# Kernel tuning notes

Measured on AMD Instinct MI355X. Metric: run time of the kernel, lower is better.

Reference implementation:

```python
import jax, jax.numpy as jnp
import numpy as np

MD_R = 64          # low-rank R
NMF_STEPS = 7      # EVAL_STEPS
INV_T = 1.0
EPS = 1e-6
GN_GROUPS = 32


def _nmf_step(x, bases, coef):
    # x: (B,D,N), bases: (B,D,R), coef: (B,N,R) -- multiplicative NMF updates
    btb = jnp.einsum('bdr,bdk->brk', bases, bases)                 # (B,R,R)
    coef = coef * jnp.einsum('bdn,bdr->bnr', x, bases) / (
        jnp.einsum('bnr,brk->bnk', coef, btb) + EPS)
    ctc = jnp.einsum('bnr,bnk->brk', coef, coef)                   # (B,R,R)
    bases = bases * jnp.einsum('bdn,bnr->bdr', x, coef) / (
        jnp.einsum('bdr,brk->bdk', bases, ctc) + EPS)
    return bases, coef


def setup_inputs() -> dict:
    key = jax.random.key(0)
    ks = jax.random.split(key, 7)
    B, C, H, W = 8, 256, 64, 64
    x = jax.random.normal(ks[0], (B, C, H, W), jnp.float32)
    w_in = jax.random.normal(ks[1], (C, C), jnp.float32) * 0.02
    b_in = jnp.zeros((C,), jnp.float32)
    w_out = jax.random.normal(ks[2], (C, C), jnp.float32) * 0.02
    gn_gamma = jnp.ones((C,), jnp.float32)
    gn_beta = jnp.zeros((C,), jnp.float32)
    bases_init = jax.random.uniform(ks[3], (B, C, MD_R), jnp.float32)  # RAND_INIT bases
    return {"x": x, "w_in": w_in, "b_in": b_in, "w_out": w_out,
            "gn_gamma": gn_gamma, "gn_beta": gn_beta, "bases_init": bases_init}


def reference(x, w_in, b_in, w_out, gn_gamma, gn_beta, bases_init):
    B, C, H, W = x.shape
    N = H * W
    # ham_in: 1x1 conv with bias, then relu
    h = jnp.einsum('bchw,oc->bohw', x, w_in) + b_in[None, :, None, None]
    h = jax.nn.relu(h)
    # NMF2D: flatten spatial (SPATIAL=True, S=1 -> D=C)
    xm = h.reshape(B, C, N)                                         # (B,D,N)
    # F.normalize(rand bases, dim=1)
    bases = bases_init / jnp.maximum(
        jnp.linalg.norm(bases_init, axis=1, keepdims=True), 1e-12)
    # local_inference runs under no_grad in the original; math identical here
    xs = jax.lax.stop_gradient(xm)
    coef = jax.nn.softmax(INV_T * jnp.einsum('bdn,bdr->bnr', xs, bases), axis=-1)
    for _ in range(NMF_STEPS):
        bases, coef = _nmf_step(xs, bases, coef)
    bases = jax.lax.stop_gradient(bases)
    coef = jax.lax.stop_gradient(coef)
    # compute_coef (differentiable w.r.t. xm)
    btb = jnp.einsum('bdr,bdk->brk', bases, bases)
    coef = coef * jnp.einsum('bdn,bdr->bnr', xm, bases) / (
        jnp.einsum('bnr,brk->bnk', coef, btb) + EPS)
    rec = jnp.einsum('bdr,bnr->bdn', bases, coef).reshape(B, C, H, W)
    # ham_out: 1x1 conv (no bias) + GroupNorm(32)
    o = jnp.einsum('bchw,oc->bohw', rec, w_out)
    g = o.reshape(B, GN_GROUPS, C // GN_GROUPS, H, W)
    mu = g.mean(axis=(2, 3, 4), keepdims=True)
    var = g.var(axis=(2, 3, 4), keepdims=True)
    g = (g - mu) * jax.lax.rsqrt(var + 1e-5)
    o = g.reshape(B, C, H, W) * gn_gamma[None, :, None, None] + gn_beta[None, :, None, None]
    # residual + relu
    return jax.nn.relu(x + o)
```

## Files before the change

kernel.cpp:

```cpp
#include <hip/hip_runtime.h>

#define B_ 8
#define C_ 256
#define N_ 4096
#define R_ 64
#define STEPS_ 7
#define NCH_ 128
#define NSP_ 32
#define EPS_ 1e-6f

typedef unsigned short u16;
typedef short bf8v __attribute__((ext_vector_type(8)));
typedef float f4v __attribute__((ext_vector_type(4)));

#define MFMA(a, b, c) __builtin_amdgcn_mfma_f32_16x16x32_bf16((a), (b), (c), 0, 0, 0)

__device__ __forceinline__ u16 bf(float x) {
  union { float f; unsigned u; } v; v.f = x;
  return (u16)((v.u + 0x7FFFu + ((v.u >> 16) & 1u)) >> 16);
}
__device__ __forceinline__ float bf2f(u16 x) {
  union { unsigned u; float f; } v; v.u = (unsigned)x << 16; return v.f;
}
__device__ __forceinline__ bf8v ldf(const u16* p) { return *(const bf8v*)p; }

__global__ __launch_bounds__(256)
void prep_kernel(const float* __restrict__ binit, float* __restrict__ bases,
                 u16* __restrict__ basesT,
                 const float* __restrict__ w1, const float* __restrict__ w2,
                 u16* __restrict__ w1b, u16* __restrict__ w2b) {
  const int t = threadIdx.x;
  if (blockIdx.x >= 8) {
    const int i = (blockIdx.x - 8) * 256 + t;
    w1b[i] = bf(w1[i]);
    w2b[i] = bf(w2[i]);
    return;
  }
  const int b = blockIdx.x;
  const int rr = t & 63, dq = t >> 6;
  const float* src = binit + (size_t)b * C_ * R_;
  float* dst = bases + (size_t)b * C_ * R_;
  u16* dT  = basesT + (size_t)b * R_ * C_;
  float vals[64];
  float s = 0.f;
#pragma unroll
  for (int i = 0; i < 64; ++i) {
    float v = src[(size_t)(dq + 4 * i) * R_ + rr];
    vals[i] = v; s = fmaf(v, v, s);
  }
  __shared__ float red[4][64];
  red[dq][rr] = s;
  __syncthreads();
  float nrm = fmaxf(sqrtf(red[0][rr] + red[1][rr] + red[2][rr] + red[3][rr]), 1e-12f);
  const float inv = 1.f / nrm;
#pragma unroll
  for (int i = 0; i < 64; ++i) {
    const int d = dq + 4 * i;
    const float v = vals[i] * inv;
    dst[(size_t)d * R_ + rr] = v;
    dT[(size_t)rr * C_ + d]  = bf(v);
  }
}

__global__ __launch_bounds__(256)
void xpose_kernel(const float* __restrict__ x, u16* __restrict__ xT) {
  const int n0 = blockIdx.x * 64, c0 = blockIdx.y * 64, b = blockIdx.z;
  __shared__ float lds[64][65];
  const int t = threadIdx.x;
  const float* xb = x + (size_t)b * C_ * N_;
  const int row = t >> 4, col4 = (t & 15) * 4;
#pragma unroll
  for (int p = 0; p < 4; ++p) {
    float4 v = *(const float4*)&xb[(size_t)(c0 + row + 16 * p) * N_ + n0 + col4];
    lds[row + 16 * p][col4 + 0] = v.x; lds[row + 16 * p][col4 + 1] = v.y;
    lds[row + 16 * p][col4 + 2] = v.z; lds[row + 16 * p][col4 + 3] = v.w;
  }
  __syncthreads();
  const int r = t >> 2, cb = (t & 3) * 16;
  __align__(16) u16 tmp[16];
#pragma unroll
  for (int j = 0; j < 16; ++j) tmp[j] = bf(lds[cb + j][r]);
  u16* o = xT + (size_t)b * N_ * C_ + (size_t)(n0 + r) * C_ + c0 + cb;
  *(uint4*)o = *(uint4*)tmp;
  *(uint4*)(o + 8) = *(uint4*)(tmp + 8);
}

__global__ __launch_bounds__(256)
void conv1_kernel(const u16* __restrict__ A, const u16* __restrict__ W,
                  const float* __restrict__ bias, u16* __restrict__ h_dn,
                  u16* __restrict__ h_nd) {
  const int nb0 = blockIdx.x * 128, ob0 = blockIdx.y * 128, b = blockIdx.z;
  const int t = threadIdx.x, w = t >> 6, lane = t & 63, g = lane >> 4, c = lane & 15;
  const int n_base = nb0 + (w >> 1) * 64, o_base = ob0 + (w & 1) * 64;
  const u16* Ab = A + (size_t)b * N_ * C_;
  f4v acc[4][4] = {};
  for (int k0 = 0; k0 < C_; k0 += 32) {
    bf8v av[4], wv[4];
#pragma unroll
    for (int mi = 0; mi < 4; ++mi)
      av[mi] = ldf(Ab + (size_t)(n_base + mi * 16 + c) * C_ + k0 + g * 8);
#pragma unroll
    for (int nj = 0; nj < 4; ++nj)
      wv[nj] = ldf(W + (size_t)(o_base + nj * 16 + c) * C_ + k0 + g * 8);
#pragma unroll
    for (int mi = 0; mi < 4; ++mi)
#pragma unroll
      for (int nj = 0; nj < 4; ++nj)
        acc[mi][nj] = MFMA(av[mi], wv[nj], acc[mi][nj]);
  }
  __shared__ float lds[64][65];
  for (int p = 0; p < 4; ++p) {
    if (w == p) {
#pragma unroll
      for (int mi = 0; mi < 4; ++mi)
#pragma unroll
        for (int nj = 0; nj < 4; ++nj) {
          const float bb = bias[o_base + nj * 16 + c];
#pragma unroll
          for (int rg = 0; rg < 4; ++rg)
            lds[mi * 16 + g * 4 + rg][nj * 16 + c] = fmaxf(acc[mi][nj][rg] + bb, 0.f);
        }
    }
    __syncthreads();
    const int pn = nb0 + (p >> 1) * 64, po = ob0 + (p & 1) * 64;
    {
      const int n = t >> 2, ob2 = (t & 3) * 16;
      __align__(16) u16 tmp[16];
#pragma unroll
      for (int j = 0; j < 16; ++j) tmp[j] = bf(lds[n][ob2 + j]);
      u16* o = h_nd + (size_t)b * N_ * C_ + (size_t)(pn + n) * C_ + po + ob2;
      *(uint4*)o = *(uint4*)tmp; *(uint4*)(o + 8) = *(uint4*)(tmp + 8);
    }
    {
      const int oo = t >> 2, nb2 = (t & 3) * 16;
      __align__(16) u16 tmp[16];
#pragma unroll
      for (int j = 0; j < 16; ++j) tmp[j] = bf(lds[nb2 + j][oo]);
      u16* o = h_dn + (size_t)b * C_ * N_ + (size_t)(po + oo) * N_ + pn + nb2;
      *(uint4*)o = *(uint4*)tmp; *(uint4*)(o + 8) = *(uint4*)(tmp + 8);
    }
    __syncthreads();
  }
}

template<int MODE>
__global__ __launch_bounds__(512)
void nmf_kernel(const u16* __restrict__ h_nd, const u16* __restrict__ h_dn,
                const u16* __restrict__ basesT, const u16* __restrict__ w2b,
                u16* __restrict__ coef_bf, u16* __restrict__ m2_bf,
                float* __restrict__ ctcp, float* __restrict__ xcp) {
  const int nc0 = blockIdx.x * NCH_;
  const int b = blockIdx.y;
  const int t = threadIdx.x, w = t >> 6, lane = t & 63, g = lane >> 4, c = lane & 15;
  __shared__ u16 bT_s[64 * 256];
  __shared__ u16 btb_s[64][72];
  __shared__ u16 coef_s[128][72];
  __shared__ u16 coefT_s[64][136];
  const u16* hb = h_nd + (size_t)b * N_ * C_;
  const u16* bT = basesT + (size_t)b * R_ * C_;
  u16* cb = coef_bf + (size_t)b * N_ * R_;

#pragma unroll
  for (int i = 0; i < 4; ++i) {
    const int lin = t + i * 512;
    const int r = lin >> 5, k = lin & 31;
    *(uint4*)&bT_s[r * 256 + ((k ^ (r & 7)) * 8)] =
        *(const uint4*)&bT[(size_t)r * C_ + k * 8];
  }
  if (MODE != 0) {
    const int row = t >> 2, seg = (t & 3) * 16;
    const u16* src = cb + (size_t)(nc0 + row) * R_ + seg;
    *(uint4*)&coef_s[row][seg] = *(const uint4*)src;
    *(uint4*)&coef_s[row][seg + 8] = *(const uint4*)(src + 8);
  }
  __syncthreads();

  const int nl = w * 16 + c;

  f4v num[4] = {}, bt[4] = {};
  const u16* An = hb + (size_t)(nc0 + nl) * C_;
  for (int k0 = 0; k0 < C_; k0 += 32) {
    const int kc = (k0 >> 3) + g;
    bf8v bv[4];
#pragma unroll
    for (int nj = 0; nj < 4; ++nj)
      bv[nj] = *(const bf8v*)&bT_s[(nj * 16 + c) * 256 + ((kc ^ (c & 7)) * 8)];
    bf8v a = ldf(An + k0 + g * 8);
#pragma unroll
    for (int nj = 0; nj < 4; ++nj) num[nj] = MFMA(a, bv[nj], num[nj]);
    if (w < 4) {
      bf8v a2 = *(const bf8v*)&bT_s[(w * 16 + c) * 256 + ((kc ^ (c & 7)) * 8)];
#pragma unroll
      for (int nj = 0; nj < 4; ++nj) bt[nj] = MFMA(a2, bv[nj], bt[nj]);
    }
  }

  if (MODE == 0) {
#pragma unroll
    for (int rg = 0; rg < 4; ++rg) {
      float m = fmaxf(fmaxf(num[0][rg], num[1][rg]), fmaxf(num[2][rg], num[3][rg]));
#pragma unroll
      for (int off = 1; off < 16; off <<= 1) m = fmaxf(m, __shfl_xor(m, off));
      float e[4], s = 0.f;
#pragma unroll
      for (int nj = 0; nj < 4; ++nj) { e[nj] = __expf(num[nj][rg] - m); s += e[nj]; }
#pragma unroll
      for (int off = 1; off < 16; off <<= 1) s += __shfl_xor(s, off);
      const float inv = 1.f / s;
#pragma unroll
      for (int nj = 0; nj < 4; ++nj)
        coef_s[w * 16 + g * 4 + rg][nj * 16 + c] = bf(e[nj] * inv);
    }
  }

  if (w < 4) {
#pragma unroll
    for (int nj = 0; nj < 4; ++nj)
#pragma unroll
      for (int rg = 0; rg < 4; ++rg)
        btb_s[w * 16 + g * 4 + rg][nj * 16 + c] = bf(bt[nj][rg]);
  }
  __syncthreads();

  f4v den[4] = {};
#pragma unroll
  for (int k0 = 0; k0 < R_; k0 += 32) {
    bf8v a = *(const bf8v*)&coef_s[nl][k0 + g * 8];
#pragma unroll
    for (int nj = 0; nj < 4; ++nj)
      den[nj] = MFMA(a, *(const bf8v*)&btb_s[nj * 16 + c][k0 + g * 8], den[nj]);
  }
  __syncthreads();

#pragma unroll
  for (int nj = 0; nj < 4; ++nj)
#pragma unroll
    for (int rg = 0; rg < 4; ++rg) {
      const int row = w * 16 + g * 4 + rg, r = nj * 16 + c;
      const float old = bf2f(coef_s[row][r]);
      const u16 nv = bf(old * num[nj][rg] / (den[nj][rg] + EPS_));
      coef_s[row][r] = nv;
      if (MODE <= 1) coefT_s[r][row] = nv;
    }
  __syncthreads();

  {
    const int row = t >> 2, seg = (t & 3) * 16;
    u16* dst = cb + (size_t)(nc0 + row) * R_ + seg;
    *(uint4*)dst = *(const uint4*)&coef_s[row][seg];
    *(uint4*)(dst + 8) = *(const uint4*)&coef_s[row][seg + 8];
  }

  if (MODE <= 1) {
    f4v xa[2][4] = {};
    const u16* hd = h_dn + (size_t)b * C_ * N_;
    for (int k0 = 0; k0 < NCH_; k0 += 32) {
      bf8v bv[4];
#pragma unroll
      for (int nj = 0; nj < 4; ++nj)
        bv[nj] = *(const bf8v*)&coefT_s[nj * 16 + c][k0 + g * 8];
#pragma unroll
      for (int mi = 0; mi < 2; ++mi) {
        bf8v a = ldf(hd + (size_t)(w * 32 + mi * 16 + c) * N_ + nc0 + k0 + g * 8);
#pragma unroll
        for (int nj = 0; nj < 4; ++nj) xa[mi][nj] = MFMA(a, bv[nj], xa[mi][nj]);
      }
    }
    float* xo = xcp + ((size_t)b * NSP_ + blockIdx.x) * (C_ * R_);
#pragma unroll
    for (int mi = 0; mi < 2; ++mi)
#pragma unroll
      for (int nj = 0; nj < 4; ++nj)
#pragma unroll
        for (int rg = 0; rg < 4; ++rg)
          xo[(size_t)(w * 32 + mi * 16 + g * 4 + rg) * R_ + nj * 16 + c] = xa[mi][nj][rg];
    if (w < 4) {
      f4v ca[4] = {};
      for (int k0 = 0; k0 < NCH_; k0 += 32) {
        bf8v a = *(const bf8v*)&coefT_s[w * 16 + c][k0 + g * 8];
#pragma unroll
        for (int nj = 0; nj < 4; ++nj)
          ca[nj] = MFMA(a, *(const bf8v*)&coefT_s[nj * 16 + c][k0 + g * 8], ca[nj]);
      }
      float* co = ctcp + ((size_t)b * NSP_ + blockIdx.x) * (R_ * R_);
#pragma unroll
      for (int nj = 0; nj < 4; ++nj)
#pragma unroll
        for (int rg = 0; rg < 4; ++rg)
          co[(size_t)(w * 16 + g * 4 + rg) * R_ + nj * 16 + c] = ca[nj][rg];
    }
  }

  if (MODE == 2 && blockIdx.x == 0) {
    f4v ma[2][4] = {};
    for (int k0 = 0; k0 < C_; k0 += 32) {
      const int kc = (k0 >> 3) + g;
      bf8v bv[4];
#pragma unroll
      for (int nj = 0; nj < 4; ++nj)
        bv[nj] = *(const bf8v*)&bT_s[(nj * 16 + c) * 256 + ((kc ^ (c & 7)) * 8)];
#pragma unroll
      for (int mi = 0; mi < 2; ++mi) {
        bf8v a = ldf(w2b + (size_t)(w * 32 + mi * 16 + c) * C_ + k0 + g * 8);
#pragma unroll
        for (int nj = 0; nj < 4; ++nj) ma[mi][nj] = MFMA(a, bv[nj], ma[mi][nj]);
      }
    }
    u16* mo = m2_bf + (size_t)b * C_ * R_;
#pragma unroll
    for (int mi = 0; mi < 2; ++mi)
#pragma unroll
      for (int nj = 0; nj < 4; ++nj)
#pragma unroll
        for (int rg = 0; rg < 4; ++rg)
          mo[(size_t)(w * 32 + mi * 16 + g * 4 + rg) * R_ + nj * 16 + c] = bf(ma[mi][nj][rg]);
  }
}

__global__ __launch_bounds__(256)
void bases_update_kernel(const float* __restrict__ xcp, const float* __restrict__ ctcp,
                         float* __restrict__ bases, u16* __restrict__ basesT) {
  const int dt = blockIdx.x & 3, rt = blockIdx.x >> 2, b = blockIdx.y;
  const int d0 = dt * 64, rb = rt * 16;
  float* bb = bases + (size_t)b * C_ * R_;
  __shared__ float ctc_s[64][16];
  __shared__ float b_s[64][65];
  const int t = threadIdx.x;
  {
    const int k = t >> 2, cr = (t & 3) * 4;
    float4 a = make_float4(0, 0, 0, 0);
    for (int s = 0; s < NSP_; ++s) {
      float4 v = *(const float4*)&ctcp[((size_t)b * NSP_ + s) * (R_ * R_) + (size_t)k * R_ + rb + cr];
      a.x += v.x; a.y += v.y; a.z += v.z; a.w += v.w;
    }
    *(float4*)&ctc_s[k][cr] = a;
  }
  {
    const int lc = t & 63, lr = t >> 6;
#pragma unroll
    for (int p = 0; p < 16; ++p)
      b_s[lr + 4 * p][lc] = bb[(size_t)(d0 + lr + 4 * p) * R_ + lc];
  }
  __syncthreads();
  const int dd = t >> 2, r0 = rb + (t & 3) * 4, cr = (t & 3) * 4;
  float4 num2 = make_float4(0, 0, 0, 0);
  for (int s = 0; s < NSP_; ++s) {
    float4 v = *(const float4*)&xcp[(((size_t)b * NSP_ + s) * C_ + d0 + dd) * R_ + r0];
    num2.x += v.x; num2.y += v.y; num2.z += v.z; num2.w += v.w;
  }
  float4 den = make_float4(0, 0, 0, 0);
#pragma unroll
  for (int k = 0; k < 64; ++k) {
    const float a = b_s[dd][k];
    float4 cv = *(const float4*)&ctc_s[k][cr];
    den.x = fmaf(a, cv.x, den.x); den.y = fmaf(a, cv.y, den.y);
    den.z = fmaf(a, cv.z, den.z); den.w = fmaf(a, cv.w, den.w);
  }
  float4 o;
  o.x = b_s[dd][r0 + 0] * num2.x / (den.x + EPS_);
  o.y = b_s[dd][r0 + 1] * num2.y / (den.y + EPS_);
  o.z = b_s[dd][r0 + 2] * num2.z / (den.z + EPS_);
  o.w = b_s[dd][r0 + 3] * num2.w / (den.w + EPS_);
  *(float4*)&bb[(size_t)(d0 + dd) * R_ + r0] = o;
  u16* oT = basesT + (size_t)b * R_ * C_ + d0 + dd;
  oT[(size_t)(r0 + 0) * C_] = bf(o.x); oT[(size_t)(r0 + 1) * C_] = bf(o.y);
  oT[(size_t)(r0 + 2) * C_] = bf(o.z); oT[(size_t)(r0 + 3) * C_] = bf(o.w);
}

__global__ __launch_bounds__(256)
void conv2_kernel(const u16* __restrict__ coef, const u16* __restrict__ m2,
                  float* __restrict__ of32, float* __restrict__ pstats) {
  const int nb0 = blockIdx.x * 128, ob0 = blockIdx.y * 128, b = blockIdx.z;
  const int t = threadIdx.x, w = t >> 6, lane = t & 63, g = lane >> 4, c = lane & 15;
  const int n_base = nb0 + (w >> 1) * 64, o_base = ob0 + (w & 1) * 64;
  const u16* Ab = coef + (size_t)b * N_ * R_;
  const u16* Wb = m2 + (size_t)b * C_ * R_;
  f4v acc[4][4] = {};
#pragma unroll
  for (int k0 = 0; k0 < R_; k0 += 32) {
    bf8v av[4], wv[4];
#pragma unroll
    for (int mi = 0; mi < 4; ++mi)
      av[mi] = ldf(Ab + (size_t)(n_base + mi * 16 + c) * R_ + k0 + g * 8);
#pragma unroll
    for (int nj = 0; nj < 4; ++nj)
      wv[nj] = ldf(Wb + (size_t)(o_base + nj * 16 + c) * R_ + k0 + g * 8);
#pragma unroll
    for (int mi = 0; mi < 4; ++mi)
#pragma unroll
      for (int nj = 0; nj < 4; ++nj)
        acc[mi][nj] = MFMA(av[mi], wv[nj], acc[mi][nj]);
  }
  __shared__ float lds[64][65];
  float sacc0 = 0.f, sacc1 = 0.f, s2acc0 = 0.f, s2acc1 = 0.f;
  for (int p = 0; p < 4; ++p) {
    if (w == p) {
#pragma unroll
      for (int mi = 0; mi < 4; ++mi)
#pragma unroll
        for (int nj = 0; nj < 4; ++nj)
#pragma unroll
          for (int rg = 0; rg < 4; ++rg)
            lds[mi * 16 + g * 4 + rg][nj * 16 + c] = acc[mi][nj][rg];
    }
    __syncthreads();
    const int pn = nb0 + (p >> 1) * 64, po = ob0 + (p & 1) * 64;
    const int oo = t >> 2, nb2 = (t & 3) * 16;
    float* o = of32 + (size_t)b * C_ * N_ + (size_t)(po + oo) * N_ + pn + nb2;
    float ls = 0.f, ls2 = 0.f;
#pragma unroll
    for (int q = 0; q < 4; ++q) {
      float4 v = make_float4(lds[nb2 + q * 4 + 0][oo], lds[nb2 + q * 4 + 1][oo],
                             lds[nb2 + q * 4 + 2][oo], lds[nb2 + q * 4 + 3][oo]);
      *(float4*)&o[q * 4] = v;
      ls += v.x + v.y + v.z + v.w;
      ls2 = fmaf(v.x, v.x, ls2); ls2 = fmaf(v.y, v.y, ls2);
      ls2 = fmaf(v.z, v.z, ls2); ls2 = fmaf(v.w, v.w, ls2);
    }
    if ((p & 1) == 0) { sacc0 += ls; s2acc0 += ls2; }
    else              { sacc1 += ls; s2acc1 += ls2; }
    __syncthreads();
  }
  {
    const int oo = t >> 2, q4 = t & 3;
    lds[oo][q4] = sacc0;      lds[oo][4 + q4] = s2acc0;
    lds[oo][8 + q4] = sacc1;  lds[oo][12 + q4] = s2acc1;
    __syncthreads();
    if (t < 128) {
      const int hh = t >> 6, oo2 = t & 63;
      const int base = hh * 8;
      float s = lds[oo2][base] + lds[oo2][base + 1] + lds[oo2][base + 2] + lds[oo2][base + 3];
      float s2 = lds[oo2][base + 4] + lds[oo2][base + 5] + lds[oo2][base + 6] + lds[oo2][base + 7];
      float* ps = pstats + (((size_t)blockIdx.z * 32 + blockIdx.x) * 256 +
                            (size_t)blockIdx.y * 128 + hh * 64 + oo2) * 2;
      ps[0] = s; ps[1] = s2;
    }
  }
}

__global__ __launch_bounds__(256)
void gn_final_kernel(const float* __restrict__ x, const float* __restrict__ gamma,
                     const float* __restrict__ beta, const float* __restrict__ pstats,
                     float* __restrict__ out) {
  const int t = threadIdx.x;
  const size_t gid0 = (size_t)blockIdx.x * 256;
  const size_t idx0 = gid0 * 4;
  const int b = (int)(idx0 >> 20);
  const int c = (int)((idx0 & ((1u << 20) - 1)) >> 12);
  const int g = c >> 3;
  float s, s2;
  {
    const int nb = t >> 3, ch = g * 8 + (t & 7);
    const float* ps = pstats + (((size_t)b * 32 + nb) * 256 + ch) * 2;
    s = ps[0]; s2 = ps[1];
  }
#pragma unroll
  for (int off = 32; off > 0; off >>= 1) { s += __shfl_down(s, off); s2 += __shfl_down(s2, off); }
  __shared__ float rs[4], rs2[4], fin[2];
  if ((t & 63) == 0) { rs[t >> 6] = s; rs2[t >> 6] = s2; }
  __syncthreads();
  if (t == 0) {
    float S = rs[0] + rs[1] + rs[2] + rs[3];
    float S2 = rs2[0] + rs2[1] + rs2[2] + rs2[3];
    float mean = S / 32768.f;
    float var = S2 / 32768.f - mean * mean;
    fin[0] = mean; fin[1] = rsqrtf(var + 1e-5f);
  }
  __syncthreads();
  const float mean = fin[0], rstd = fin[1];
  const float ga = gamma[c] * rstd;
  const float be = beta[c] - mean * ga;
  const size_t gid = gid0 + t;
  float4 ov = ((const float4*)out)[gid];
  float4 xv = ((const float4*)x)[gid];
  float4 r;
  r.x = fmaxf(fmaf(ov.x, ga, be) + xv.x, 0.f);
  r.y = fmaxf(fmaf(ov.y, ga, be) + xv.y, 0.f);
  r.z = fmaxf(fmaf(ov.z, ga, be) + xv.z, 0.f);
  r.w = fmaxf(fmaf(ov.w, ga, be) + xv.w, 0.f);
  ((float4*)out)[gid] = r;
}

extern "C" void kernel_launch(void* const* d_in, const int* in_sizes, int n_in,
                              void* d_out, int out_size, void* d_ws, size_t ws_size,
                              hipStream_t stream) {
  (void)in_sizes; (void)n_in; (void)out_size; (void)ws_size;
  const float* x     = (const float*)d_in[0];
  const float* w_in  = (const float*)d_in[1];
  const float* b_in  = (const float*)d_in[2];
  const float* w_out = (const float*)d_in[3];
  const float* gamma = (const float*)d_in[4];
  const float* beta  = (const float*)d_in[5];
  const float* binit = (const float*)d_in[6];
  float* out = (float*)d_out;

  float* p = (float*)d_ws;
  u16* xT = (u16*)p;        p += 4194304;
  u16* h_nd = (u16*)p;      p += 4194304;
  u16* h_dn = (u16*)p;      p += 4194304;
  u16* coef_bf = (u16*)p;   p += 1048576;
  float* bases = p;         p += 131072;
  u16* basesT = (u16*)p;    p += 65536;
  u16* m2_bf = (u16*)p;     p += 65536;
  float* ctcp = p;          p += 1048576;
  float* xcp = p;           p += 4194304;
  u16* w1b = (u16*)p;       p += 32768;
  u16* w2b = (u16*)p;       p += 32768;
  float* pstats = p;        p += 131072;

  prep_kernel<<<dim3(264), 256, 0, stream>>>(binit, bases, basesT, w_in, w_out, w1b, w2b);
  xpose_kernel<<<dim3(64, 4, 8), 256, 0, stream>>>(x, xT);
  conv1_kernel<<<dim3(32, 2, 8), 256, 0, stream>>>(xT, w1b, b_in, h_dn, h_nd);

  nmf_kernel<0><<<dim3(32, 8), 512, 0, stream>>>(h_nd, h_dn, basesT, w2b, coef_bf,
                                                 m2_bf, ctcp, xcp);
  bases_update_kernel<<<dim3(16, 8), 256, 0, stream>>>(xcp, ctcp, bases, basesT);
  for (int it = 1; it < STEPS_; ++it) {
    nmf_kernel<1><<<dim3(32, 8), 512, 0, stream>>>(h_nd, h_dn, basesT, w2b, coef_bf,
                                                   m2_bf, ctcp, xcp);
    bases_update_kernel<<<dim3(16, 8), 256, 0, stream>>>(xcp, ctcp, bases, basesT);
  }
  nmf_kernel<2><<<dim3(32, 8), 512, 0, stream>>>(h_nd, h_dn, basesT, w2b, coef_bf,
                                                 m2_bf, ctcp, xcp);
  conv2_kernel<<<dim3(32, 2, 8), 256, 0, stream>>>(coef_bf, m2_bf, out, pstats);
  gn_final_kernel<<<dim3((B_ * C_ * N_) / 4 / 256), 256, 0, stream>>>(x, gamma, beta,
                                                                      pstats, out);
}
```

Measured before the change: 272.0 us.

## Fuse input transpose into conv1 and store bases partials in bf16

Drops the separate transpose kernel. conv1 now reads fp32 x directly, converts it to bf16 and transposes it into shared memory one k-slice at a time. It also changes the per-chunk partial sums of x·coef (xcp) from fp32 to bf16, halving the traffic that the bases update writes and reads every NMF iteration. The trade-off is extra syncs and scalar LDS stores with possible bank conflicts inside conv1, and lower precision when the 32 partials are summed.

```diff
diff --git a/kernel.cpp b/kernel.cpp
--- a/kernel.cpp
+++ b/kernel.cpp
@@ -63,42 +63,37 @@
 }
 
 __global__ __launch_bounds__(256)
-void xpose_kernel(const float* __restrict__ x, u16* __restrict__ xT) {
-  const int n0 = blockIdx.x * 64, c0 = blockIdx.y * 64, b = blockIdx.z;
-  __shared__ float lds[64][65];
-  const int t = threadIdx.x;
-  const float* xb = x + (size_t)b * C_ * N_;
-  const int row = t >> 4, col4 = (t & 15) * 4;
-#pragma unroll
-  for (int p = 0; p < 4; ++p) {
-    float4 v = *(const float4*)&xb[(size_t)(c0 + row + 16 * p) * N_ + n0 + col4];
-    lds[row + 16 * p][col4 + 0] = v.x; lds[row + 16 * p][col4 + 1] = v.y;
-    lds[row + 16 * p][col4 + 2] = v.z; lds[row + 16 * p][col4 + 3] = v.w;
-  }
-  __syncthreads();
-  const int r = t >> 2, cb = (t & 3) * 16;
-  __align__(16) u16 tmp[16];
-#pragma unroll
-  for (int j = 0; j < 16; ++j) tmp[j] = bf(lds[cb + j][r]);
-  u16* o = xT + (size_t)b * N_ * C_ + (size_t)(n0 + r) * C_ + c0 + cb;
-  *(uint4*)o = *(uint4*)tmp;
-  *(uint4*)(o + 8) = *(uint4*)(tmp + 8);
-}
-
-__global__ __launch_bounds__(256)
-void conv1_kernel(const u16* __restrict__ A, const u16* __restrict__ W,
+void conv1_kernel(const float* __restrict__ x, const u16* __restrict__ W,
                   const float* __restrict__ bias, u16* __restrict__ h_dn,
                   u16* __restrict__ h_nd) {
   const int nb0 = blockIdx.x * 128, ob0 = blockIdx.y * 128, b = blockIdx.z;
   const int t = threadIdx.x, w = t >> 6, lane = t & 63, g = lane >> 4, c = lane & 15;
-  const int n_base = nb0 + (w >> 1) * 64, o_base = ob0 + (w & 1) * 64;
-  const u16* Ab = A + (size_t)b * N_ * C_;
+  const int nloc = (w >> 1) * 64, o_base = ob0 + (w & 1) * 64;
+  const float* xb = x + (size_t)b * C_ * N_ + nb0;
+  __shared__ u16 xa_s[128][40];
+  __shared__ float lds[64][65];
+  const int skk = t >> 3, sn = (t & 7) * 16;
   f4v acc[4][4] = {};
   for (int k0 = 0; k0 < C_; k0 += 32) {
+    if (k0) __syncthreads();
+    const float* src = &xb[(size_t)(k0 + skk) * N_ + sn];
+    float4 v0 = *(const float4*)src;
+    float4 v1 = *(const float4*)(src + 4);
+    float4 v2 = *(const float4*)(src + 8);
+    float4 v3 = *(const float4*)(src + 12);
+    xa_s[sn + 0][skk] = bf(v0.x);  xa_s[sn + 1][skk] = bf(v0.y);
+    xa_s[sn + 2][skk] = bf(v0.z);  xa_s[sn + 3][skk] = bf(v0.w);
+    xa_s[sn + 4][skk] = bf(v1.x);  xa_s[sn + 5][skk] = bf(v1.y);
+    xa_s[sn + 6][skk] = bf(v1.z);  xa_s[sn + 7][skk] = bf(v1.w);
+    xa_s[sn + 8][skk] = bf(v2.x);  xa_s[sn + 9][skk] = bf(v2.y);
+    xa_s[sn + 10][skk] = bf(v2.z); xa_s[sn + 11][skk] = bf(v2.w);
+    xa_s[sn + 12][skk] = bf(v3.x); xa_s[sn + 13][skk] = bf(v3.y);
+    xa_s[sn + 14][skk] = bf(v3.z); xa_s[sn + 15][skk] = bf(v3.w);
+    __syncthreads();
     bf8v av[4], wv[4];
 #pragma unroll
     for (int mi = 0; mi < 4; ++mi)
-      av[mi] = ldf(Ab + (size_t)(n_base + mi * 16 + c) * C_ + k0 + g * 8);
+      av[mi] = *(const bf8v*)&xa_s[nloc + mi * 16 + c][g * 8];
 #pragma unroll
     for (int nj = 0; nj < 4; ++nj)
       wv[nj] = ldf(W + (size_t)(o_base + nj * 16 + c) * C_ + k0 + g * 8);
@@ -108,7 +103,7 @@
       for (int nj = 0; nj < 4; ++nj)
         acc[mi][nj] = MFMA(av[mi], wv[nj], acc[mi][nj]);
   }
-  __shared__ float lds[64][65];
+  __syncthreads();
   for (int p = 0; p < 4; ++p) {
     if (w == p) {
 #pragma unroll
@@ -148,7 +143,7 @@
 void nmf_kernel(const u16* __restrict__ h_nd, const u16* __restrict__ h_dn,
                 const u16* __restrict__ basesT, const u16* __restrict__ w2b,
                 u16* __restrict__ coef_bf, u16* __restrict__ m2_bf,
-                float* __restrict__ ctcp, float* __restrict__ xcp) {
+                float* __restrict__ ctcp, u16* __restrict__ xcp) {
   const int nc0 = blockIdx.x * NCH_;
   const int b = blockIdx.y;
   const int t = threadIdx.x, w = t >> 6, lane = t & 63, g = lane >> 4, c = lane & 15;
@@ -266,14 +261,14 @@
         for (int nj = 0; nj < 4; ++nj) xa[mi][nj] = MFMA(a, bv[nj], xa[mi][nj]);
       }
     }
-    float* xo = xcp + ((size_t)b * NSP_ + blockIdx.x) * (C_ * R_);
+    u16* xo = xcp + ((size_t)b * NSP_ + blockIdx.x) * (C_ * R_);
 #pragma unroll
     for (int mi = 0; mi < 2; ++mi)
 #pragma unroll
       for (int nj = 0; nj < 4; ++nj)
 #pragma unroll
         for (int rg = 0; rg < 4; ++rg)
-          xo[(size_t)(w * 32 + mi * 16 + g * 4 + rg) * R_ + nj * 16 + c] = xa[mi][nj][rg];
+          xo[(size_t)(w * 32 + mi * 16 + g * 4 + rg) * R_ + nj * 16 + c] = bf(xa[mi][nj][rg]);
     if (w < 4) {
       f4v ca[4] = {};
       for (int k0 = 0; k0 < NCH_; k0 += 32) {
@@ -318,7 +313,7 @@
 }
 
 __global__ __launch_bounds__(256)
-void bases_update_kernel(const float* __restrict__ xcp, const float* __restrict__ ctcp,
+void bases_update_kernel(const u16* __restrict__ xcp, const float* __restrict__ ctcp,
                          float* __restrict__ bases, u16* __restrict__ basesT) {
   const int dt = blockIdx.x & 3, rt = blockIdx.x >> 2, b = blockIdx.y;
   const int d0 = dt * 64, rb = rt * 16;
@@ -345,8 +340,9 @@
   const int dd = t >> 2, r0 = rb + (t & 3) * 4, cr = (t & 3) * 4;
   float4 num2 = make_float4(0, 0, 0, 0);
   for (int s = 0; s < NSP_; ++s) {
-    float4 v = *(const float4*)&xcp[(((size_t)b * NSP_ + s) * C_ + d0 + dd) * R_ + r0];
-    num2.x += v.x; num2.y += v.y; num2.z += v.z; num2.w += v.w;
+    ushort4 v = *(const ushort4*)&xcp[(((size_t)b * NSP_ + s) * C_ + d0 + dd) * R_ + r0];
+    num2.x += bf2f(v.x); num2.y += bf2f(v.y);
+    num2.z += bf2f(v.z); num2.w += bf2f(v.w);
   }
   float4 den = make_float4(0, 0, 0, 0);
 #pragma unroll
@@ -495,7 +491,6 @@
   float* out = (float*)d_out;
 
   float* p = (float*)d_ws;
-  u16* xT = (u16*)p;        p += 4194304;
   u16* h_nd = (u16*)p;      p += 4194304;
   u16* h_dn = (u16*)p;      p += 4194304;
   u16* coef_bf = (u16*)p;   p += 1048576;
@@ -503,14 +498,13 @@
   u16* basesT = (u16*)p;    p += 65536;
   u16* m2_bf = (u16*)p;     p += 65536;
   float* ctcp = p;          p += 1048576;
-  float* xcp = p;           p += 4194304;
+  u16* xcp = (u16*)p;       p += 2097152;
   u16* w1b = (u16*)p;       p += 32768;
   u16* w2b = (u16*)p;       p += 32768;
   float* pstats = p;        p += 131072;
 
   prep_kernel<<<dim3(264), 256, 0, stream>>>(binit, bases, basesT, w_in, w_out, w1b, w2b);
-  xpose_kernel<<<dim3(64, 4, 8), 256, 0, stream>>>(x, xT);
-  conv1_kernel<<<dim3(32, 2, 8), 256, 0, stream>>>(xT, w1b, b_in, h_dn, h_nd);
+  conv1_kernel<<<dim3(32, 2, 8), 256, 0, stream>>>(x, w1b, b_in, h_dn, h_nd);
 
   nmf_kernel<0><<<dim3(32, 8), 512, 0, stream>>>(h_nd, h_dn, basesT, w2b, coef_bf,
                                                  m2_bf, ctcp, xcp);
```

After: 254.1 us, median of 3. 6.6% less time.
